# Kernel tuning notes

Measured on AMD Instinct MI355X. Metric: run time of the kernel, lower is better.

The kernel has to match this reference:

```python
import jax, jax.numpy as jnp
import numpy as np

DIM = 384
NHEAD = 8
HD = DIM // NHEAD          # 48, rotary/pos-enc head dim
P = 3
CORR_DIM = 2 * 49 * P * P  # 882
NFRAMES = 24
PPI = 96                   # patches per frame
NPATCH = NFRAMES * PPI     # 2304 SoftAgg segments (unique kk)
E = NPATCH * NFRAMES       # 55296 edges
M = PPI                    # tokens per (i,j) group


def _linear(x, W, b):
    return x @ W + b


def _ln(x, g, b, eps=1e-3):
    mu = x.mean(-1, keepdims=True)
    var = ((x - mu) ** 2).mean(-1, keepdims=True)
    return (x - mu) * jax.lax.rsqrt(var + eps) * g + b


def _mlp2(x, W1, b1, W2, b2):
    return _linear(jax.nn.relu(_linear(x, W1, b1)), W2, b2)


@jax.custom_vjp
def grad_clip(x):
    return x

def _gc_fwd(x):
    return x, None

def _gc_bwd(_, g):
    g = jnp.where(jnp.isnan(g), jnp.zeros_like(g), g)
    return (jnp.clip(g, -0.01, 0.01),)

grad_clip.defvjp(_gc_fwd, _gc_bwd)


def _soft_agg(x, seg, Wf, bf, Wg, bg, Wh, bh):
    # x: [1,E,D]; seg: [E] contiguous segment ids in [0, NPATCH)
    g = _linear(x, Wg, bg)[0]                                    # [E,D]
    gmax = jax.ops.segment_max(g, seg, num_segments=NPATCH)
    ex = jnp.exp(g - gmax[seg])
    den = jax.ops.segment_sum(ex, seg, num_segments=NPATCH)
    w = ex / den[seg]                                            # scatter_softmax over segments
    f = _linear(x, Wf, bf)[0]
    y = jax.ops.segment_sum(f * w, seg, num_segments=NPATCH)     # [NPATCH,D]
    return _linear(y, Wh, bh)[seg][None]                         # expand back to [1,E,D]


def _rotate_half(x):
    x1, x2 = jnp.split(x, 2, axis=-1)
    return jnp.concatenate([-x2, x1], axis=-1)


def _gated_linear_attention(x, cos, sin, Wq, bq, Wk, bk, Wv, bv, Wm, bm, Wgt, bgt):
    # x: [N,M,D]; cos/sin: [N,1,M,HD] broadcast over heads
    N = x.shape[0]
    def heads(t):
        return t.reshape(N, M, NHEAD, HD).transpose(0, 2, 1, 3)  # [N,H,M,HD]
    q = heads(_linear(x, Wq, bq))
    k = heads(_linear(x, Wk, bk))
    v = heads(_linear(x, Wv, bv))
    q = q * cos + _rotate_half(q) * sin
    k = k * cos + _rotate_half(k) * sin
    Q = jax.nn.elu(q) + 1.0
    K = jax.nn.elu(k) + 1.0
    KV = jnp.einsum('nhsd,nhsv->nhdv', K, v)
    Z = 1.0 / (jnp.einsum('nhld,nhd->nhl', Q, K.sum(2)) + 1e-6)
    out = jnp.einsum('nhld,nhdv,nhl->nhlv', Q, KV, Z)
    msg = _linear(out.transpose(0, 2, 1, 3).reshape(N, M, DIM), Wm, bm)
    gate = jax.nn.sigmoid(_linear(jnp.concatenate([x, msg], -1), Wgt, bgt))
    return x + gate * msg


def _forward(net, inp, corr, posenc_cache, kk, ix, jx, ij_ind,
             Wc1, bc1, Wc2, bc2, g_lnc, b_lnc, Wc3, bc3,
             g_norm, b_norm,
             W1a, b1a, W1b, b1b, W2a, b2a, W2b, b2b,
             Wf, bf, Wg, bg, Wh, bh,
             g_norm2, b_norm2,
             Wq, bq, Wk, bk, Wv, bv, Wm, bm, Wgt, bgt,
             Wd, bd, Ww, bw):
    # corr encoder: Linear-ReLU-Linear-LN-ReLU-Linear
    c = jax.nn.relu(_linear(corr, Wc1, bc1))
    c = _ln(_linear(c, Wc2, bc2), g_lnc, b_lnc)
    c = _linear(jax.nn.relu(c), Wc3, bc3)
    net = net + inp + c
    net = _ln(net, g_norm, b_norm)
    # neighbor gather + masked MLP + residual (mask applied BEFORE the MLP, as in torch)
    mask_ix = (ix >= 0).astype(net.dtype)[None, :, None]
    mask_jx = (jx >= 0).astype(net.dtype)[None, :, None]
    net = net + _mlp2(mask_ix * net[:, ix], W1a, b1a, W1b, b1b)
    net = net + _mlp2(mask_jx * net[:, jx], W2a, b2a, W2b, b2b)
    net = net + _soft_agg(net, kk, Wf, bf, Wg, bg, Wh, bh)
    b = net.shape[0]
    flat = ij_ind.reshape(-1)
    tokens = net[:, flat, :].reshape(-1, M, DIM)                 # [N,M,D], N = E//M
    pe = posenc_cache[:, :, :, flat, :].reshape(2, tokens.shape[0], 1, M, HD)
    tokens = _ln(tokens, g_norm2, b_norm2)
    tokens = _gated_linear_attention(tokens, pe[0], pe[1], Wq, bq, Wk, bk, Wv, bv, Wm, bm, Wgt, bgt)
    tokens = tokens.reshape(b, -1, DIM)
    reverse_ind = jnp.zeros((E,), jnp.int32).at[flat].set(jnp.arange(E, dtype=jnp.int32))
    net = tokens[:, reverse_ind, :]
    d_out = grad_clip(_linear(jax.nn.relu(net), Wd, bd))
    w_out = jax.nn.sigmoid(grad_clip(_linear(jax.nn.relu(net), Ww, bw)))
    return net, d_out, w_out


def setup_inputs() -> dict:
    key = jax.random.key(0)
    ki = iter(jax.random.split(key, 80))
    # complete patch graph: each patch connects to all frames; edge id = k*NFRAMES + j
    kkn = np.repeat(np.arange(NPATCH), NFRAMES)
    iin = kkn // PPI
    jjn = np.tile(np.arange(NFRAMES), NPATCH)
    e = np.arange(E)
    ixn = np.where(jjn >= 1, e - 1, -1)                 # fastba.neighbors: same kk, jj-1
    jxn = np.where(jjn + 1 < NFRAMES, e + 1, -1)        # same kk, jj+1
    ij = iin * 12345 + jjn
    ij_ind = np.sort(np.argsort(ij, kind='stable').reshape(-1, M), axis=-1)

    def rn(shape):
        return jax.random.normal(next(ki), shape, jnp.float32)
    def W(fi, fo):
        s = 1.0 / np.sqrt(fi)
        return jax.random.uniform(next(ki), (fi, fo), jnp.float32, -s, s)
    def bvec(fi, n):
        s = 1.0 / np.sqrt(fi)
        return jax.random.uniform(next(ki), (n,), jnp.float32, -s, s)

    theta = jax.random.uniform(next(ki), (1, 1, E, HD), jnp.float32, 0.0, 2.0 * np.pi)
    posenc = jnp.stack([jnp.cos(theta), jnp.sin(theta)], axis=0)  # [2,1,1,E,HD]

    return {
        'net': rn((1, E, DIM)), 'inp': rn((1, E, DIM)),
        'corr': rn((1, E, CORR_DIM)), 'flow': rn((1, E, 2)),
        'posenc_cache': posenc,
        'ii': jnp.asarray(iin, jnp.int32), 'jj': jnp.asarray(jjn, jnp.int32),
        'kk': jnp.asarray(kkn, jnp.int32), 'ix': jnp.asarray(ixn, jnp.int32),
        'jx': jnp.asarray(jxn, jnp.int32), 'ij_ind': jnp.asarray(ij_ind, jnp.int32),
        'Wc1': W(CORR_DIM, DIM), 'bc1': bvec(CORR_DIM, DIM),
        'Wc2': W(DIM, DIM), 'bc2': bvec(DIM, DIM),
        'g_lnc': jnp.ones((DIM,), jnp.float32), 'b_lnc': jnp.zeros((DIM,), jnp.float32),
        'Wc3': W(DIM, DIM), 'bc3': bvec(DIM, DIM),
        'g_norm': jnp.ones((DIM,), jnp.float32), 'b_norm': jnp.zeros((DIM,), jnp.float32),
        'W1a': W(DIM, DIM), 'b1a': bvec(DIM, DIM), 'W1b': W(DIM, DIM), 'b1b': bvec(DIM, DIM),
        'W2a': W(DIM, DIM), 'b2a': bvec(DIM, DIM), 'W2b': W(DIM, DIM), 'b2b': bvec(DIM, DIM),
        'Wf': W(DIM, DIM), 'bf': bvec(DIM, DIM), 'Wg': W(DIM, DIM), 'bg': bvec(DIM, DIM),
        'Wh': W(DIM, DIM), 'bh': bvec(DIM, DIM),
        'g_norm2': jnp.ones((DIM,), jnp.float32), 'b_norm2': jnp.zeros((DIM,), jnp.float32),
        'Wq': W(DIM, DIM), 'bq': bvec(DIM, DIM), 'Wk': W(DIM, DIM), 'bk': bvec(DIM, DIM),
        'Wv': W(DIM, DIM), 'bv': bvec(DIM, DIM), 'Wm': W(DIM, DIM), 'bm': bvec(DIM, DIM),
        'Wgt': W(2 * DIM, DIM), 'bgt': bvec(2 * DIM, DIM),
        'Wd': W(DIM, 2), 'bd': bvec(DIM, 2), 'Ww': W(DIM, 2), 'bw': bvec(DIM, 2),
    }


def reference(net, inp, corr, flow, posenc_cache, ii, jj, kk, ix, jx, ij_ind,
              Wc1, bc1, Wc2, bc2, g_lnc, b_lnc, Wc3, bc3,
              g_norm, b_norm,
              W1a, b1a, W1b, b1b, W2a, b2a, W2b, b2b,
              Wf, bf, Wg, bg, Wh, bh,
              g_norm2, b_norm2,
              Wq, bq, Wk, bk, Wv, bv, Wm, bm, Wgt, bgt,
              Wd, bd, Ww, bw):
    return _forward(net, inp, corr, posenc_cache, kk, ix, jx, ij_ind,
                    Wc1, bc1, Wc2, bc2, g_lnc, b_lnc, Wc3, bc3,
                    g_norm, b_norm,
                    W1a, b1a, W1b, b1b, W2a, b2a, W2b, b2b,
                    Wf, bf, Wg, bg, Wh, bh,
                    g_norm2, b_norm2,
                    Wq, bq, Wk, bk, Wv, bv, Wm, bm, Wgt, bgt,
                    Wd, bd, Ww, bw)
```

## Files before the change

### kernel.cpp

```cpp
#include <hip/hip_runtime.h>
#include <math.h>

#define DIMV 384
#define NHEADV 8
#define HDV 48
#define CORR_DIMV 882
#define CORR_PAD 896
#define NFRAMESV 24
#define PPIV 96
#define NPATCHV (NFRAMESV * PPIV)
#define ETOK (NPATCHV * NFRAMESV)
#define MTOK 96
#define NGRP (ETOK / MTOK)

using f32x4 = __attribute__((ext_vector_type(4))) float;
using s16x8 = __attribute__((ext_vector_type(8))) short;
using u16x4 = __attribute__((ext_vector_type(4))) unsigned short;

__device__ __forceinline__ unsigned int f2bf(float x) {
    union { float f; unsigned int u; } c; c.f = x;
    unsigned int u = c.u;
    u += 0x7fffu + ((u >> 16) & 1u);
    return u >> 16;
}
__device__ __forceinline__ float bf2f(unsigned short x) {
    union { unsigned int u; float f; } c; c.u = ((unsigned int)x) << 16;
    return c.f;
}

__device__ __forceinline__ void gload_lds16(const void* g, void* l) {
    __builtin_amdgcn_global_load_lds(
        (const __attribute__((address_space(1))) unsigned int*)g,
        (__attribute__((address_space(3))) unsigned int*)l, 16, 0, 0);
}

__device__ __forceinline__ void xcd_tile(int& colblk, int& rowblk) {
    const int nwg  = gridDim.x * gridDim.y;
    const int flat = blockIdx.y * gridDim.x + blockIdx.x;
    const int xcd  = flat & 7;
    const int base = flat >> 3;
    const int q = nwg >> 3, r = nwg & 7;
    const int nf = (xcd < r ? xcd * (q + 1) : r * (q + 1) + (xcd - r) * q) + base;
    colblk = nf % gridDim.x;
    rowblk = nf / gridDim.x;
}

template<int EPI, bool GATHER>
__global__ __launch_bounds__(256)
void gemm_bb(const unsigned short* __restrict__ A, int lda,
             const unsigned short* __restrict__ Wt,
             const float* __restrict__ bias,
             float* __restrict__ C,
             unsigned short* __restrict__ Cb, int ldcb, int cbofs,
             const int* __restrict__ gidx,
             const unsigned short* __restrict__ zrow, int K)
{
    int colblk, rowblk;
    xcd_tile(colblk, rowblk);
    const int row0 = rowblk * 128;
    const int col0 = colblk * 128;

    __shared__ __align__(16) unsigned short As[128 * 32];
    __shared__ __align__(16) unsigned short Bs[128 * 32];

    const int tid  = threadIdx.x;
    const int lane = tid & 63;
    const int wid  = tid >> 6;
    const int wm   = wid >> 1;
    const int wn   = wid & 1;

    const int rl = lane >> 2;
    const int cp = lane & 3;

    const unsigned short* asrc[2];
    const unsigned short* bsrc[2];
    #pragma unroll
    for (int s = 0; s < 2; ++s) {
        const int r = wid * 32 + s * 16 + rl;
        const int c = cp ^ ((r >> 1) & 3);
        long arow = row0 + r;
        if (GATHER) arow = gidx[row0 + r];
        asrc[s] = (GATHER && arow < 0) ? (zrow + c * 8)
                                       : (A + arow * (long)lda + c * 8);
        bsrc[s] = Wt + (long)(col0 + r) * K + c * 8;
    }
    unsigned short* adst[2] = { &As[(wid * 32) * 32], &As[(wid * 32 + 16) * 32] };
    unsigned short* bdst[2] = { &Bs[(wid * 32) * 32], &Bs[(wid * 32 + 16) * 32] };

    f32x4 acc[4][4] = {};
    const int ntiles = K >> 5;

    for (int t = 0; t < ntiles; ++t) {
        const int ko = t * 32;
        gload_lds16(asrc[0] + ko, adst[0]);
        gload_lds16(asrc[1] + ko, adst[1]);
        gload_lds16(bsrc[0] + ko, bdst[0]);
        gload_lds16(bsrc[1] + ko, bdst[1]);
        __syncthreads();

        const int rsel = lane & 15;
        const int kq   = lane >> 4;
        s16x8 a[4], b[4];
        #pragma unroll
        for (int i = 0; i < 4; ++i) {
            const int R = wm * 64 + i * 16 + rsel;
            a[i] = *(const s16x8*)&As[R * 32 + ((kq ^ ((R >> 1) & 3)) << 3)];
        }
        #pragma unroll
        for (int j = 0; j < 4; ++j) {
            const int R = wn * 64 + j * 16 + rsel;
            b[j] = *(const s16x8*)&Bs[R * 32 + ((kq ^ ((R >> 1) & 3)) << 3)];
        }
        #pragma unroll
        for (int i = 0; i < 4; ++i)
            #pragma unroll
            for (int j = 0; j < 4; ++j)
                acc[i][j] = __builtin_amdgcn_mfma_f32_16x16x32_bf16(a[i], b[j], acc[i][j], 0, 0, 0);
        __syncthreads();
    }

    const int ccol = lane & 15;
    const int rgrp = lane >> 4;
    #pragma unroll
    for (int i = 0; i < 4; ++i) {
        const long rbase = row0 + wm * 64 + i * 16 + rgrp * 4;
        #pragma unroll
        for (int j = 0; j < 4; ++j) {
            const int col = col0 + wn * 64 + j * 16 + ccol;
            const float bsv = bias ? bias[col] : 0.f;
            #pragma unroll
            for (int rr = 0; rr < 4; ++rr) {
                const long row = rbase + rr;
                float v = acc[i][j][rr] + bsv;
                if (EPI == 0) C[row * (long)DIMV + col] = v;
                if (EPI == 1) Cb[row * (long)ldcb + cbofs + col] = (unsigned short)f2bf(fmaxf(v, 0.f));
                if (EPI == 3) { const long off = row * (long)DIMV + col;
                                const float nv = C[off] + v;
                                C[off] = nv; Cb[row * (long)ldcb + col] = (unsigned short)f2bf(nv); }
                if (EPI == 5) Cb[row * (long)ldcb + cbofs + col] = (unsigned short)f2bf(v);
                if (EPI == 7) {
                    const float gate = 1.f / (1.f + expf(-v));
                    const float tok  = bf2f(Cb[row * (long)ldcb + col]);
                    const float msg  = bf2f(Cb[row * (long)ldcb + cbofs + col]);
                    C[(long)gidx[row] * DIMV + col] = tok + gate * msg;
                }
            }
        }
    }
}

struct WPtrs13 { const float* p[13]; };

__global__ __launch_bounds__(256)
void wtrans13(WPtrs13 w, unsigned short* __restrict__ out)
{
    __shared__ float t[32][33];
    const float* W = w.p[blockIdx.z];
    unsigned short* O = out + (size_t)blockIdx.z * DIMV * DIMV;
    const int k0 = blockIdx.x * 32, n0 = blockIdx.y * 32;
    const int tx = threadIdx.x, ty = threadIdx.y;
    #pragma unroll
    for (int i = ty; i < 32; i += 8)
        t[i][tx] = W[(long)(k0 + i) * DIMV + n0 + tx];
    __syncthreads();
    #pragma unroll
    for (int i = ty; i < 32; i += 8)
        O[(long)(n0 + i) * DIMV + k0 + tx] = (unsigned short)f2bf(t[tx][i]);
}

__global__ __launch_bounds__(256)
void wtransb(const float* __restrict__ W, unsigned short* __restrict__ O,
             int krows, int ldo)
{
    __shared__ float t[32][33];
    const int k0 = blockIdx.x * 32, n0 = blockIdx.y * 32;
    const int tx = threadIdx.x, ty = threadIdx.y;
    #pragma unroll
    for (int i = ty; i < 32; i += 8)
        t[i][tx] = (k0 + i < krows) ? W[(long)(k0 + i) * DIMV + n0 + tx] : 0.f;
    __syncthreads();
    #pragma unroll
    for (int i = ty; i < 32; i += 8)
        O[(long)(n0 + i) * ldo + k0 + tx] = (unsigned short)f2bf(t[tx][i]);
}

__global__ __launch_bounds__(256)
void corrconv(const float* __restrict__ corr, unsigned int* __restrict__ corrb,
              unsigned int* __restrict__ zr)
{
    if (blockIdx.x == 0 && threadIdx.x < 512) zr[threadIdx.x] = 0u;
    const long idx = (long)blockIdx.x * 256 + threadIdx.x;
    if (idx >= (long)ETOK * (CORR_PAD / 2)) return;
    const long e = idx / (CORR_PAD / 2);
    const int  p = (int)(idx % (CORR_PAD / 2));
    const int  k = p * 2;
    unsigned v = 0u;
    if (k + 1 < CORR_DIMV) {
        const float2 f = *(const float2*)(corr + e * CORR_DIMV + k);
        v = f2bf(f.x) | (f2bf(f.y) << 16);
    }
    corrb[idx] = v;
}

template<int MODE, bool RELUB>
__global__ __launch_bounds__(256)
void ln_kernel(float* __restrict__ dst, unsigned short* __restrict__ dstb, int ldb,
               const float* __restrict__ s0, const float* __restrict__ s1,
               const unsigned short* __restrict__ sb,
               const float* __restrict__ seg, const int* __restrict__ gather,
               const float* __restrict__ g, const float* __restrict__ b)
{
    const int wave = threadIdx.x >> 6;
    const int lane = threadIdx.x & 63;
    const long row = (long)blockIdx.x * 4 + wave;
    const long srow = (MODE == 2) ? (long)gather[row] : row;

    float x[6];
    float sum = 0.f;
    #pragma unroll
    for (int i = 0; i < 6; ++i) {
        int c = lane + i * 64;
        float v;
        if (MODE == 0) v = bf2f(sb[srow * DIMV + c]);
        if (MODE == 1) v = s0[srow * DIMV + c] + s1[srow * DIMV + c] + bf2f(sb[srow * DIMV + c]);
        if (MODE == 2) v = s0[srow * DIMV + c] + seg[(srow / NFRAMESV) * DIMV + c];
        x[i] = v; sum += v;
    }
    #pragma unroll
    for (int o = 32; o > 0; o >>= 1) sum += __shfl_xor(sum, o);
    float mu = sum * (1.f / DIMV);
    float vs = 0.f;
    #pragma unroll
    for (int i = 0; i < 6; ++i) { float d = x[i] - mu; vs += d * d; }
    #pragma unroll
    for (int o = 32; o > 0; o >>= 1) vs += __shfl_xor(vs, o);
    float rstd = rsqrtf(vs * (1.f / DIMV) + 1e-3f);
    #pragma unroll
    for (int i = 0; i < 6; ++i) {
        int c = lane + i * 64;
        float y = (x[i] - mu) * rstd * g[c] + b[c];
        if (dst)  dst[row * DIMV + c] = y;
        if (dstb) dstb[row * (long)ldb + c] =
            (unsigned short)f2bf(RELUB ? fmaxf(y, 0.f) : y);
    }
}

__global__ __launch_bounds__(384)
void softagg_kernel(const unsigned short* __restrict__ gbuf,
                    const unsigned short* __restrict__ fbuf,
                    unsigned short* __restrict__ yb)
{
    const int p = blockIdx.x;
    const int col = threadIdx.x;
    const long base = (long)p * NFRAMESV * DIMV + col;
    float gv[NFRAMESV];
    float gmax = -INFINITY;
    #pragma unroll
    for (int r = 0; r < NFRAMESV; ++r) {
        gv[r] = bf2f(gbuf[base + (long)r * DIMV]);
        gmax = fmaxf(gmax, gv[r]);
    }
    float den = 0.f;
    #pragma unroll
    for (int r = 0; r < NFRAMESV; ++r) { gv[r] = expf(gv[r] - gmax); den += gv[r]; }
    float acc = 0.f;
    #pragma unroll
    for (int r = 0; r < NFRAMESV; ++r) acc += bf2f(fbuf[base + (long)r * DIMV]) * gv[r];
    yb[(long)p * DIMV + col] = (unsigned short)f2bf(acc / den);
}

__global__ __launch_bounds__(256)
void rope_kernel(unsigned short* __restrict__ q, unsigned short* __restrict__ k,
                 const float* __restrict__ pos, const int* __restrict__ flat)
{
    const long idx = (long)blockIdx.x * 256 + threadIdx.x;
    const long e = idx / 48;
    const int rem = (int)(idx % 48);
    const int h = rem / 6, d4 = (rem % 6) * 4;
    const int tok = flat[e];
    const float* cp = pos + (long)tok * HDV;
    const float* sp = pos + (long)ETOK * HDV + (long)tok * HDV;
    const float4 c1 = *(const float4*)(cp + d4);
    const float4 c2 = *(const float4*)(cp + d4 + 24);
    const float4 s1 = *(const float4*)(sp + d4);
    const float4 s2 = *(const float4*)(sp + d4 + 24);
    const long o1 = e * DIMV + h * HDV + d4;
    const long o2 = o1 + 24;

    float c1a[4] = {c1.x, c1.y, c1.z, c1.w};
    float c2a[4] = {c2.x, c2.y, c2.z, c2.w};
    float s1a[4] = {s1.x, s1.y, s1.z, s1.w};
    float s2a[4] = {s2.x, s2.y, s2.z, s2.w};

    u16x4 q1 = *(const u16x4*)&q[o1];
    u16x4 q2 = *(const u16x4*)&q[o2];
    u16x4 k1 = *(const u16x4*)&k[o1];
    u16x4 k2 = *(const u16x4*)&k[o2];
    u16x4 q1o, q2o, k1o, k2o;
    #pragma unroll
    for (int i = 0; i < 4; ++i) {
        const float qa = bf2f(q1[i]), qb = bf2f(q2[i]);
        float r1 = qa * c1a[i] - qb * s1a[i];
        float r2 = qb * c2a[i] + qa * s2a[i];
        r1 = (r1 > 0.f) ? r1 + 1.f : expf(r1);
        r2 = (r2 > 0.f) ? r2 + 1.f : expf(r2);
        q1o[i] = (unsigned short)f2bf(r1);
        q2o[i] = (unsigned short)f2bf(r2);
        const float ka = bf2f(k1[i]), kb = bf2f(k2[i]);
        float t1 = ka * c1a[i] - kb * s1a[i];
        float t2 = kb * c2a[i] + ka * s2a[i];
        t1 = (t1 > 0.f) ? t1 + 1.f : expf(t1);
        t2 = (t2 > 0.f) ? t2 + 1.f : expf(t2);
        k1o[i] = (unsigned short)f2bf(t1);
        k2o[i] = (unsigned short)f2bf(t2);
    }
    *(u16x4*)&q[o1] = q1o;
    *(u16x4*)&q[o2] = q2o;
    *(u16x4*)&k[o1] = k1o;
    *(u16x4*)&k[o2] = k2o;
}

__global__ __launch_bounds__(256)
void attn_kernel(const unsigned short* __restrict__ qb,
                 const unsigned short* __restrict__ kb,
                 const unsigned short* __restrict__ vb,
                 unsigned short* __restrict__ ob)
{
    __shared__ unsigned short KVt[4][48][64];
    __shared__ float KsumS[4][48];
    __shared__ float ZlS[4][96];

    const int tid  = threadIdx.x;
    const int wid  = tid >> 6;
    const int lane = tid & 63;
    const int task = blockIdx.x * 4 + wid;
    const int n = task >> 3, h = task & 7;

    const long base = ((long)n * MTOK) * DIMV + h * HDV;

    const int c16   = lane & 15;
    const int kq    = lane >> 4;
    const int khalf = kq * 8;

    if (lane < 48) {
        const int s = (lane & 7) << 3;
        const uint4 z = make_uint4(0u, 0u, 0u, 0u);
        *(uint4*)&KVt[wid][lane][48 ^ s] = z;
        *(uint4*)&KVt[wid][lane][56 ^ s] = z;
    }

    f32x4 kv[3][3] = {};
    float ksum_p[3] = {0.f, 0.f, 0.f};

    for (int ks = 0; ks < 3; ++ks) {
        const int l0 = ks * 32 + khalf;
        s16x8 afr[3], bfr[3];
        #pragma unroll
        for (int mf = 0; mf < 3; ++mf) {
            const int d = mf * 16 + c16;
            union { unsigned short us[8]; s16x8 v; } pk;
            float s = 0.f;
            #pragma unroll
            for (int j = 0; j < 8; ++j) {
                const unsigned short kw = kb[base + (long)(l0 + j) * DIMV + d];
                s += bf2f(kw);
                pk.us[j] = kw;
            }
            ksum_p[mf] += s;
            afr[mf] = pk.v;
        }
        #pragma unroll
        for (int nf = 0; nf < 3; ++nf) {
            const int dv = nf * 16 + c16;
            union { unsigned short us[8]; s16x8 v; } pk;
            #pragma unroll
            for (int j = 0; j < 8; ++j)
                pk.us[j] = vb[base + (long)(l0 + j) * DIMV + dv];
            bfr[nf] = pk.v;
        }
        #pragma unroll
        for (int mf = 0; mf < 3; ++mf)
            #pragma unroll
            for (int nf = 0; nf < 3; ++nf)
                kv[mf][nf] = __builtin_amdgcn_mfma_f32_16x16x32_bf16(afr[mf], bfr[nf], kv[mf][nf], 0, 0, 0);
    }

    #pragma unroll
    for (int mf = 0; mf < 3; ++mf) {
        float s = ksum_p[mf];
        s += __shfl_xor(s, 16);
        s += __shfl_xor(s, 32);
        if (kq == 0) KsumS[wid][mf * 16 + c16] = s;
    }

    #pragma unroll
    for (int mf = 0; mf < 3; ++mf) {
        #pragma unroll
        for (int nf = 0; nf < 3; ++nf) {
            const int dv = nf * 16 + c16;
            const int d0 = (mf * 16 + kq * 4) ^ ((dv & 7) << 3);
            uint2 w;
            w.x = f2bf(kv[mf][nf][0]) | (f2bf(kv[mf][nf][1]) << 16);
            w.y = f2bf(kv[mf][nf][2]) | (f2bf(kv[mf][nf][3]) << 16);
            *(uint2*)&KVt[wid][dv][d0] = w;
        }
    }

    s16x8 qf[6][2];
    const s16x8 zfrag = {0, 0, 0, 0, 0, 0, 0, 0};
    #pragma unroll
    for (int mf = 0; mf < 6; ++mf) {
        const int l = mf * 16 + c16;
        float dsum = 0.f;
        #pragma unroll
        for (int ks = 0; ks < 2; ++ks) {
            if (ks == 0 || kq < 2) {
                const int d = ks * 32 + khalf;
                union { unsigned short us[8]; s16x8 v; } pk;
                pk.v = *(const s16x8*)&qb[base + (long)l * DIMV + d];
                #pragma unroll
                for (int j = 0; j < 8; ++j)
                    dsum += bf2f(pk.us[j]) * KsumS[wid][d + j];
                qf[mf][ks] = pk.v;
            } else {
                qf[mf][ks] = zfrag;
            }
        }
        dsum += __shfl_xor(dsum, 16);
        dsum += __shfl_xor(dsum, 32);
        if (kq == 0) ZlS[wid][l] = 1.f / (dsum + 1e-6f);
    }

    #pragma unroll
    for (int nf = 0; nf < 3; ++nf) {
        const int dv = nf * 16 + c16;
        const int sw = (dv & 7) << 3;
        const s16x8 b0 = *(const s16x8*)&KVt[wid][dv][khalf ^ sw];
        const s16x8 b1 = *(const s16x8*)&KVt[wid][dv][(32 + khalf) ^ sw];
        #pragma unroll
        for (int mf = 0; mf < 6; ++mf) {
            f32x4 a = {};
            a = __builtin_amdgcn_mfma_f32_16x16x32_bf16(qf[mf][0], b0, a, 0, 0, 0);
            a = __builtin_amdgcn_mfma_f32_16x16x32_bf16(qf[mf][1], b1, a, 0, 0, 0);
            const int lb = mf * 16 + kq * 4;
            const long rbase = base + (long)lb * DIMV + dv;
            #pragma unroll
            for (int rr = 0; rr < 4; ++rr) {
                const float z = ZlS[wid][lb + rr];
                ob[rbase + (long)rr * DIMV] = (unsigned short)f2bf(a[rr] * z);
            }
        }
    }
}

__global__ __launch_bounds__(256)
void head_kernel(const float* __restrict__ net,
                 const float* __restrict__ Wd, const float* __restrict__ bd,
                 const float* __restrict__ Ww, const float* __restrict__ bw,
                 float* __restrict__ dout, float* __restrict__ wout)
{
    const int wave = threadIdx.x >> 6;
    const int lane = threadIdx.x & 63;
    const long row = (long)blockIdx.x * 4 + wave;
    const float* p = net + row * DIMV;
    float a0 = 0.f, a1 = 0.f, a2 = 0.f, a3 = 0.f;
    #pragma unroll
    for (int i = 0; i < 6; ++i) {
        int c = lane + i * 64;
        float r = fmaxf(p[c], 0.f);
        a0 = fmaf(r, Wd[c * 2 + 0], a0);
        a1 = fmaf(r, Wd[c * 2 + 1], a1);
        a2 = fmaf(r, Ww[c * 2 + 0], a2);
        a3 = fmaf(r, Ww[c * 2 + 1], a3);
    }
    #pragma unroll
    for (int o = 32; o > 0; o >>= 1) {
        a0 += __shfl_xor(a0, o);
        a1 += __shfl_xor(a1, o);
        a2 += __shfl_xor(a2, o);
        a3 += __shfl_xor(a3, o);
    }
    if (lane == 0) {
        dout[row * 2 + 0] = a0 + bd[0];
        dout[row * 2 + 1] = a1 + bd[1];
        wout[row * 2 + 0] = 1.f / (1.f + expf(-(a2 + bw[0])));
        wout[row * 2 + 1] = 1.f / (1.f + expf(-(a3 + bw[1])));
    }
}

extern "C" void kernel_launch(void* const* d_in, const int* in_sizes, int n_in,
                              void* d_out, int out_size, void* d_ws, size_t ws_size,
                              hipStream_t stream)
{
    const float* net_in = (const float*)d_in[0];
    const float* inp    = (const float*)d_in[1];
    const float* corr   = (const float*)d_in[2];
    const float* posenc = (const float*)d_in[4];
    const int*   ix     = (const int*)d_in[8];
    const int*   jx     = (const int*)d_in[9];
    const int*   flat   = (const int*)d_in[10];

    const float* Wc1 = (const float*)d_in[11]; const float* bc1 = (const float*)d_in[12];
    const float* Wc2 = (const float*)d_in[13]; const float* bc2 = (const float*)d_in[14];
    const float* g_lnc = (const float*)d_in[15]; const float* b_lnc = (const float*)d_in[16];
    const float* Wc3 = (const float*)d_in[17]; const float* bc3 = (const float*)d_in[18];
    const float* g_norm = (const float*)d_in[19]; const float* b_norm = (const float*)d_in[20];
    const float* W1a = (const float*)d_in[21]; const float* b1a = (const float*)d_in[22];
    const float* W1b = (const float*)d_in[23]; const float* b1b = (const float*)d_in[24];
    const float* W2a = (const float*)d_in[25]; const float* b2a = (const float*)d_in[26];
    const float* W2b = (const float*)d_in[27]; const float* b2b = (const float*)d_in[28];
    const float* Wf = (const float*)d_in[29]; const float* bff = (const float*)d_in[30];
    const float* Wg = (const float*)d_in[31]; const float* bg = (const float*)d_in[32];
    const float* Wh = (const float*)d_in[33]; const float* bh = (const float*)d_in[34];
    const float* g_norm2 = (const float*)d_in[35]; const float* b_norm2 = (const float*)d_in[36];
    const float* Wq = (const float*)d_in[37]; const float* bq = (const float*)d_in[38];
    const float* Wk = (const float*)d_in[39]; const float* bk = (const float*)d_in[40];
    const float* Wv = (const float*)d_in[41]; const float* bv = (const float*)d_in[42];
    const float* Wm = (const float*)d_in[43]; const float* bm = (const float*)d_in[44];
    const float* Wgt = (const float*)d_in[45]; const float* bgt = (const float*)d_in[46];
    const float* Wd = (const float*)d_in[47]; const float* bd = (const float*)d_in[48];
    const float* Ww = (const float*)d_in[49]; const float* bw = (const float*)d_in[50];

    const size_t EB  = (size_t)ETOK * DIMV;
    const size_t WSLOT = (size_t)DIMV * DIMV;
    char* p = (char*)d_ws;
    float* X0  = (float*)p;           p += EB * 4;
    float* Y2f = (float*)p;           p += (size_t)NPATCHV * DIMV * 4;
    unsigned short* WT = (unsigned short*)p;
    p += (13 * WSLOT + (size_t)DIMV * CORR_PAD + (size_t)DIMV * 768) * 2;
    unsigned short* ZR  = (unsigned short*)p; p += 4096;
    unsigned short* Cb0 = (unsigned short*)p; p += EB * 2;
    unsigned short* Bb  = (unsigned short*)p; p += EB * 2;
    unsigned short* Xb1 = (unsigned short*)p; p += EB * 2;
    unsigned short* Xb2 = (unsigned short*)p; p += EB * 2;
    unsigned short* TM  = (unsigned short*)p; p += (size_t)ETOK * 768 * 2;
    unsigned short* Yb  = (unsigned short*)p; p += (size_t)NPATCHV * DIMV * 2;
    unsigned short* qb  = (unsigned short*)p; p += EB * 2;
    unsigned short* kb  = (unsigned short*)p; p += EB * 2;
    unsigned short* vb  = (unsigned short*)p; p += EB * 2;
    unsigned short* corrb = qb;

    unsigned short* Wc2t = WT + 0 * WSLOT;
    unsigned short* Wc3t = WT + 1 * WSLOT;
    unsigned short* W1at = WT + 2 * WSLOT;
    unsigned short* W1bt = WT + 3 * WSLOT;
    unsigned short* W2at = WT + 4 * WSLOT;
    unsigned short* W2bt = WT + 5 * WSLOT;
    unsigned short* Wft  = WT + 6 * WSLOT;
    unsigned short* Wgt_ = WT + 7 * WSLOT;
    unsigned short* Wht  = WT + 8 * WSLOT;
    unsigned short* Wqt  = WT + 9 * WSLOT;
    unsigned short* Wkt  = WT + 10 * WSLOT;
    unsigned short* Wvt  = WT + 11 * WSLOT;
    unsigned short* Wmt  = WT + 12 * WSLOT;
    unsigned short* Wc1t = WT + 13 * WSLOT;
    unsigned short* Wgtt = Wc1t + (size_t)DIMV * CORR_PAD;

    float* out_net = (float*)d_out;
    float* out_d = out_net + EB;
    float* out_w = out_d + (size_t)ETOK * 2;

    const dim3 gB(DIMV / 128, ETOK / 128);
    const dim3 gY(DIMV / 128, NPATCHV / 128);
    const int lnBlocks = ETOK / 4;

    {
        const long tot = (long)ETOK * (CORR_PAD / 2);
        corrconv<<<(int)((tot + 255) / 256), 256, 0, stream>>>(corr, (unsigned int*)corrb, (unsigned int*)ZR);
    }
    {
        WPtrs13 w;
        w.p[0] = Wc2; w.p[1] = Wc3; w.p[2] = W1a; w.p[3] = W1b; w.p[4] = W2a;
        w.p[5] = W2b; w.p[6] = Wf;  w.p[7] = Wg;  w.p[8] = Wh;  w.p[9] = Wq;
        w.p[10] = Wk; w.p[11] = Wv; w.p[12] = Wm;
        wtrans13<<<dim3(12, 12, 13), dim3(32, 8), 0, stream>>>(w, WT);
        wtransb<<<dim3(28, 12), dim3(32, 8), 0, stream>>>(Wc1, Wc1t, CORR_DIMV, CORR_PAD);
        wtransb<<<dim3(24, 12), dim3(32, 8), 0, stream>>>(Wgt, Wgtt, 768, 768);
    }

    gemm_bb<1, false><<<gB, 256, 0, stream>>>(corrb, CORR_PAD, Wc1t, bc1, nullptr, Cb0, DIMV, 0, nullptr, ZR, CORR_PAD);
    gemm_bb<5, false><<<gB, 256, 0, stream>>>(Cb0, DIMV, Wc2t, bc2, nullptr, Xb1, DIMV, 0, nullptr, ZR, DIMV);
    ln_kernel<0, true><<<lnBlocks, 256, 0, stream>>>(nullptr, Cb0, DIMV, nullptr, nullptr, Xb1, nullptr, nullptr, g_lnc, b_lnc);
    gemm_bb<5, false><<<gB, 256, 0, stream>>>(Cb0, DIMV, Wc3t, bc3, nullptr, Xb2, DIMV, 0, nullptr, ZR, DIMV);

    ln_kernel<1, false><<<lnBlocks, 256, 0, stream>>>(X0, Bb, DIMV, net_in, inp, Xb2, nullptr, nullptr, g_norm, b_norm);

    gemm_bb<1, true><<<gB, 256, 0, stream>>>(Bb, DIMV, W1at, b1a, nullptr, Cb0, DIMV, 0, ix, ZR, DIMV);
    gemm_bb<3, false><<<gB, 256, 0, stream>>>(Cb0, DIMV, W1bt, b1b, X0, Bb, DIMV, 0, nullptr, ZR, DIMV);

    gemm_bb<1, true><<<gB, 256, 0, stream>>>(Bb, DIMV, W2at, b2a, nullptr, Cb0, DIMV, 0, jx, ZR, DIMV);
    gemm_bb<3, false><<<gB, 256, 0, stream>>>(Cb0, DIMV, W2bt, b2b, X0, Bb, DIMV, 0, nullptr, ZR, DIMV);

    gemm_bb<5, false><<<gB, 256, 0, stream>>>(Bb, DIMV, Wgt_, bg, nullptr, Xb1, DIMV, 0, nullptr, ZR, DIMV);
    gemm_bb<5, false><<<gB, 256, 0, stream>>>(Bb, DIMV, Wft, bff, nullptr, Xb2, DIMV, 0, nullptr, ZR, DIMV);
    softagg_kernel<<<NPATCHV, 384, 0, stream>>>(Xb1, Xb2, Yb);
    gemm_bb<0, false><<<gY, 256, 0, stream>>>(Yb, DIMV, Wht, bh, Y2f, nullptr, DIMV, 0, nullptr, ZR, DIMV);

    ln_kernel<2, false><<<lnBlocks, 256, 0, stream>>>(nullptr, TM, 768, X0, nullptr, nullptr, Y2f, flat, g_norm2, b_norm2);

    gemm_bb<5, false><<<gB, 256, 0, stream>>>(TM, 768, Wqt, bq, nullptr, qb, DIMV, 0, nullptr, ZR, DIMV);
    gemm_bb<5, false><<<gB, 256, 0, stream>>>(TM, 768, Wkt, bk, nullptr, kb, DIMV, 0, nullptr, ZR, DIMV);
    gemm_bb<5, false><<<gB, 256, 0, stream>>>(TM, 768, Wvt, bv, nullptr, vb, DIMV, 0, nullptr, ZR, DIMV);

    rope_kernel<<<(int)((long)ETOK * 48 / 256), 256, 0, stream>>>(qb, kb, posenc, flat);

    attn_kernel<<<NGRP * NHEADV / 4, 256, 0, stream>>>(qb, kb, vb, Cb0);

    gemm_bb<5, false><<<gB, 256, 0, stream>>>(Cb0, DIMV, Wmt, bm, nullptr, TM, 768, 384, nullptr, ZR, DIMV);

    gemm_bb<7, false><<<gB, 256, 0, stream>>>(TM, 768, Wgtt, bgt, out_net, TM, 768, 384, flat, ZR, 768);

    head_kernel<<<lnBlocks, 256, 0, stream>>>(out_net, Wd, bd, Ww, bw, out_d, out_w);
}
```

Before: 1.007 ms.

## Double-buffer GEMM LDS, fuse QKV and gate/feature GEMMs, drop fp32 residual

The GEMM main loop now uses two LDS buffers. The next K-tile's global-to-LDS loads are issued before computing on the current tile, with one barrier pair per iteration instead of a load-then-compute sync pattern. The Q/K/V projections are merged into one 1152-wide GEMM, and the gate/feature projections into one 768-wide GEMM, with concatenated biases and strided consumers. The fp32 residual buffer X0 is removed so residual updates accumulate in bf16 in place. This cuts launches, A-operand rereads and fp32 traffic, at the risk of extra bf16 rounding in the residual path.

Result: faster. 882.5 us (median of 2 runs) (-12.3%).

```diff
diff --git a/kernel.cpp b/kernel.cpp
--- a/kernel.cpp
+++ b/kernel.cpp
@@ -60,8 +60,8 @@
     const int row0 = rowblk * 128;
     const int col0 = colblk * 128;
 
-    __shared__ __align__(16) unsigned short As[128 * 32];
-    __shared__ __align__(16) unsigned short Bs[128 * 32];
+    __shared__ __align__(16) unsigned short As[2 * 128 * 32];
+    __shared__ __align__(16) unsigned short Bs[2 * 128 * 32];
 
     const int tid  = threadIdx.x;
     const int lane = tid & 63;
@@ -84,40 +84,52 @@
                                        : (A + arow * (long)lda + c * 8);
         bsrc[s] = Wt + (long)(col0 + r) * K + c * 8;
     }
-    unsigned short* adst[2] = { &As[(wid * 32) * 32], &As[(wid * 32 + 16) * 32] };
-    unsigned short* bdst[2] = { &Bs[(wid * 32) * 32], &Bs[(wid * 32 + 16) * 32] };
 
     f32x4 acc[4][4] = {};
     const int ntiles = K >> 5;
-
-    for (int t = 0; t < ntiles; ++t) {
-        const int ko = t * 32;
-        gload_lds16(asrc[0] + ko, adst[0]);
-        gload_lds16(asrc[1] + ko, adst[1]);
-        gload_lds16(bsrc[0] + ko, bdst[0]);
-        gload_lds16(bsrc[1] + ko, bdst[1]);
-        __syncthreads();
-
-        const int rsel = lane & 15;
-        const int kq   = lane >> 4;
-        s16x8 a[4], b[4];
+    const int rsel = lane & 15;
+    const int kq   = lane >> 4;
+
+    auto stage = [&](int b, int ko) {
+        unsigned short* a0 = &As[b * 4096 + wid * 1024];
+        unsigned short* b0 = &Bs[b * 4096 + wid * 1024];
+        gload_lds16(asrc[0] + ko, a0);
+        gload_lds16(asrc[1] + ko, a0 + 512);
+        gload_lds16(bsrc[0] + ko, b0);
+        gload_lds16(bsrc[1] + ko, b0 + 512);
+    };
+    auto body = [&](int b) {
+        const unsigned short* Ab = &As[b * 4096];
+        const unsigned short* Bf = &Bs[b * 4096];
+        s16x8 a[4], w[4];
         #pragma unroll
         for (int i = 0; i < 4; ++i) {
             const int R = wm * 64 + i * 16 + rsel;
-            a[i] = *(const s16x8*)&As[R * 32 + ((kq ^ ((R >> 1) & 3)) << 3)];
+            a[i] = *(const s16x8*)&Ab[R * 32 + ((kq ^ ((R >> 1) & 3)) << 3)];
         }
         #pragma unroll
         for (int j = 0; j < 4; ++j) {
             const int R = wn * 64 + j * 16 + rsel;
-            b[j] = *(const s16x8*)&Bs[R * 32 + ((kq ^ ((R >> 1) & 3)) << 3)];
+            w[j] = *(const s16x8*)&Bf[R * 32 + ((kq ^ ((R >> 1) & 3)) << 3)];
         }
         #pragma unroll
         for (int i = 0; i < 4; ++i)
             #pragma unroll
             for (int j = 0; j < 4; ++j)
-                acc[i][j] = __builtin_amdgcn_mfma_f32_16x16x32_bf16(a[i], b[j], acc[i][j], 0, 0, 0);
-        __syncthreads();
-    }
+                acc[i][j] = __builtin_amdgcn_mfma_f32_16x16x32_bf16(a[i], w[j], acc[i][j], 0, 0, 0);
+    };
+
+    stage(0, 0);
+    int cur = 0;
+    for (int t = 0; t + 1 < ntiles; ++t) {
+        stage(cur ^ 1, (t + 1) << 5);
+        asm volatile("s_waitcnt vmcnt(4)\n\ts_barrier" ::: "memory");
+        body(cur);
+        asm volatile("s_barrier" ::: "memory");
+        cur ^= 1;
+    }
+    asm volatile("s_waitcnt vmcnt(0)\n\ts_barrier" ::: "memory");
+    body(cur);
 
     const int ccol = lane & 15;
     const int rgrp = lane >> 4;
@@ -134,10 +146,9 @@
                 float v = acc[i][j][rr] + bsv;
                 if (EPI == 0) C[row * (long)DIMV + col] = v;
                 if (EPI == 1) Cb[row * (long)ldcb + cbofs + col] = (unsigned short)f2bf(fmaxf(v, 0.f));
-                if (EPI == 3) { const long off = row * (long)DIMV + col;
-                                const float nv = C[off] + v;
-                                C[off] = nv; Cb[row * (long)ldcb + col] = (unsigned short)f2bf(nv); }
                 if (EPI == 5) Cb[row * (long)ldcb + cbofs + col] = (unsigned short)f2bf(v);
+                if (EPI == 6) { const long off = row * (long)ldcb + col;
+                                Cb[off] = (unsigned short)f2bf(bf2f(Cb[off]) + v); }
                 if (EPI == 7) {
                     const float gate = 1.f / (1.f + expf(-v));
                     const float tok  = bf2f(Cb[row * (long)ldcb + col]);
@@ -202,9 +213,21 @@
     corrb[idx] = v;
 }
 
+__global__ __launch_bounds__(256)
+void biascat(const float* __restrict__ bq, const float* __restrict__ bk,
+             const float* __restrict__ bv, const float* __restrict__ bg,
+             const float* __restrict__ bf_, float* __restrict__ bqkv,
+             float* __restrict__ bgf)
+{
+    const int t = blockIdx.x * 256 + threadIdx.x;
+    if (t < 384)       { bqkv[t] = bq[t];       bgf[t] = bg[t]; }
+    else if (t < 768)  { bqkv[t] = bk[t - 384]; bgf[t] = bf_[t - 384]; }
+    else if (t < 1152) { bqkv[t] = bv[t - 768]; }
+}
+
 template<int MODE, bool RELUB>
 __global__ __launch_bounds__(256)
-void ln_kernel(float* __restrict__ dst, unsigned short* __restrict__ dstb, int ldb,
+void ln_kernel(unsigned short* __restrict__ dstb, int ldb,
                const float* __restrict__ s0, const float* __restrict__ s1,
                const unsigned short* __restrict__ sb,
                const float* __restrict__ seg, const int* __restrict__ gather,
@@ -223,7 +246,7 @@
         float v;
         if (MODE == 0) v = bf2f(sb[srow * DIMV + c]);
         if (MODE == 1) v = s0[srow * DIMV + c] + s1[srow * DIMV + c] + bf2f(sb[srow * DIMV + c]);
-        if (MODE == 2) v = s0[srow * DIMV + c] + seg[(srow / NFRAMESV) * DIMV + c];
+        if (MODE == 2) v = bf2f(sb[srow * DIMV + c]) + seg[(srow / NFRAMESV) * DIMV + c];
         x[i] = v; sum += v;
     }
     #pragma unroll
@@ -239,25 +262,22 @@
     for (int i = 0; i < 6; ++i) {
         int c = lane + i * 64;
         float y = (x[i] - mu) * rstd * g[c] + b[c];
-        if (dst)  dst[row * DIMV + c] = y;
-        if (dstb) dstb[row * (long)ldb + c] =
-            (unsigned short)f2bf(RELUB ? fmaxf(y, 0.f) : y);
+        dstb[row * (long)ldb + c] = (unsigned short)f2bf(RELUB ? fmaxf(y, 0.f) : y);
     }
 }
 
 __global__ __launch_bounds__(384)
-void softagg_kernel(const unsigned short* __restrict__ gbuf,
-                    const unsigned short* __restrict__ fbuf,
+void softagg_kernel(const unsigned short* __restrict__ gf,
                     unsigned short* __restrict__ yb)
 {
     const int p = blockIdx.x;
     const int col = threadIdx.x;
-    const long base = (long)p * NFRAMESV * DIMV + col;
+    const long base = (long)p * NFRAMESV * 768 + col;
     float gv[NFRAMESV];
     float gmax = -INFINITY;
     #pragma unroll
     for (int r = 0; r < NFRAMESV; ++r) {
-        gv[r] = bf2f(gbuf[base + (long)r * DIMV]);
+        gv[r] = bf2f(gf[base + (long)r * 768]);
         gmax = fmaxf(gmax, gv[r]);
     }
     float den = 0.f;
@@ -265,13 +285,13 @@
     for (int r = 0; r < NFRAMESV; ++r) { gv[r] = expf(gv[r] - gmax); den += gv[r]; }
     float acc = 0.f;
     #pragma unroll
-    for (int r = 0; r < NFRAMESV; ++r) acc += bf2f(fbuf[base + (long)r * DIMV]) * gv[r];
+    for (int r = 0; r < NFRAMESV; ++r) acc += bf2f(gf[base + 384 + (long)r * 768]) * gv[r];
     yb[(long)p * DIMV + col] = (unsigned short)f2bf(acc / den);
 }
 
 __global__ __launch_bounds__(256)
 void rope_kernel(unsigned short* __restrict__ q, unsigned short* __restrict__ k,
-                 const float* __restrict__ pos, const int* __restrict__ flat)
+                 int ld, const float* __restrict__ pos, const int* __restrict__ flat)
 {
     const long idx = (long)blockIdx.x * 256 + threadIdx.x;
     const long e = idx / 48;
@@ -284,7 +304,7 @@
     const float4 c2 = *(const float4*)(cp + d4 + 24);
     const float4 s1 = *(const float4*)(sp + d4);
     const float4 s2 = *(const float4*)(sp + d4 + 24);
-    const long o1 = e * DIMV + h * HDV + d4;
+    const long o1 = e * ld + h * HDV + d4;
     const long o2 = o1 + 24;
 
     float c1a[4] = {c1.x, c1.y, c1.z, c1.w};
@@ -323,8 +343,8 @@
 __global__ __launch_bounds__(256)
 void attn_kernel(const unsigned short* __restrict__ qb,
                  const unsigned short* __restrict__ kb,
-                 const unsigned short* __restrict__ vb,
-                 unsigned short* __restrict__ ob)
+                 const unsigned short* __restrict__ vb, int ld,
+                 unsigned short* __restrict__ ob, int ldo)
 {
     __shared__ unsigned short KVt[4][48][64];
     __shared__ float KsumS[4][48];
@@ -336,7 +356,8 @@
     const int task = blockIdx.x * 4 + wid;
     const int n = task >> 3, h = task & 7;
 
-    const long base = ((long)n * MTOK) * DIMV + h * HDV;
+    const long base  = ((long)n * MTOK) * ld + h * HDV;
+    const long baseo = ((long)n * MTOK) * ldo + h * HDV;
 
     const int c16   = lane & 15;
     const int kq    = lane >> 4;
@@ -362,7 +383,7 @@
             float s = 0.f;
             #pragma unroll
             for (int j = 0; j < 8; ++j) {
-                const unsigned short kw = kb[base + (long)(l0 + j) * DIMV + d];
+                const unsigned short kw = kb[base + (long)(l0 + j) * ld + d];
                 s += bf2f(kw);
                 pk.us[j] = kw;
             }
@@ -375,7 +396,7 @@
             union { unsigned short us[8]; s16x8 v; } pk;
             #pragma unroll
             for (int j = 0; j < 8; ++j)
-                pk.us[j] = vb[base + (long)(l0 + j) * DIMV + dv];
+                pk.us[j] = vb[base + (long)(l0 + j) * ld + dv];
             bfr[nf] = pk.v;
         }
         #pragma unroll
@@ -417,7 +438,7 @@
             if (ks == 0 || kq < 2) {
                 const int d = ks * 32 + khalf;
                 union { unsigned short us[8]; s16x8 v; } pk;
-                pk.v = *(const s16x8*)&qb[base + (long)l * DIMV + d];
+                pk.v = *(const s16x8*)&qb[base + (long)l * ld + d];
                 #pragma unroll
                 for (int j = 0; j < 8; ++j)
                     dsum += bf2f(pk.us[j]) * KsumS[wid][d + j];
@@ -443,11 +464,11 @@
             a = __builtin_amdgcn_mfma_f32_16x16x32_bf16(qf[mf][0], b0, a, 0, 0, 0);
             a = __builtin_amdgcn_mfma_f32_16x16x32_bf16(qf[mf][1], b1, a, 0, 0, 0);
             const int lb = mf * 16 + kq * 4;
-            const long rbase = base + (long)lb * DIMV + dv;
+            const long rbase = baseo + (long)lb * ldo + dv;
             #pragma unroll
             for (int rr = 0; rr < 4; ++rr) {
                 const float z = ZlS[wid][lb + rr];
-                ob[rbase + (long)rr * DIMV] = (unsigned short)f2bf(a[rr] * z);
+                ob[rbase + (long)rr * ldo] = (unsigned short)f2bf(a[rr] * z);
             }
         }
     }
@@ -524,21 +545,21 @@
     const size_t EB  = (size_t)ETOK * DIMV;
     const size_t WSLOT = (size_t)DIMV * DIMV;
     char* p = (char*)d_ws;
-    float* X0  = (float*)p;           p += EB * 4;
     float* Y2f = (float*)p;           p += (size_t)NPATCHV * DIMV * 4;
     unsigned short* WT = (unsigned short*)p;
     p += (13 * WSLOT + (size_t)DIMV * CORR_PAD + (size_t)DIMV * 768) * 2;
     unsigned short* ZR  = (unsigned short*)p; p += 4096;
+    float* bqkv = (float*)p;          p += 1152 * 4;
+    float* bgf  = (float*)p;          p += 768 * 4;
     unsigned short* Cb0 = (unsigned short*)p; p += EB * 2;
     unsigned short* Bb  = (unsigned short*)p; p += EB * 2;
     unsigned short* Xb1 = (unsigned short*)p; p += EB * 2;
     unsigned short* Xb2 = (unsigned short*)p; p += EB * 2;
+    unsigned short* Xgf = (unsigned short*)p; p += (size_t)ETOK * 768 * 2;
     unsigned short* TM  = (unsigned short*)p; p += (size_t)ETOK * 768 * 2;
     unsigned short* Yb  = (unsigned short*)p; p += (size_t)NPATCHV * DIMV * 2;
-    unsigned short* qb  = (unsigned short*)p; p += EB * 2;
-    unsigned short* kb  = (unsigned short*)p; p += EB * 2;
-    unsigned short* vb  = (unsigned short*)p; p += EB * 2;
-    unsigned short* corrb = qb;
+    unsigned short* QKV = (unsigned short*)p; p += (size_t)ETOK * 1152 * 2;
+    unsigned short* corrb = QKV;
 
     unsigned short* Wc2t = WT + 0 * WSLOT;
     unsigned short* Wc3t = WT + 1 * WSLOT;
@@ -546,12 +567,9 @@
     unsigned short* W1bt = WT + 3 * WSLOT;
     unsigned short* W2at = WT + 4 * WSLOT;
     unsigned short* W2bt = WT + 5 * WSLOT;
-    unsigned short* Wft  = WT + 6 * WSLOT;
-    unsigned short* Wgt_ = WT + 7 * WSLOT;
+    unsigned short* WgfT = WT + 6 * WSLOT;
     unsigned short* Wht  = WT + 8 * WSLOT;
-    unsigned short* Wqt  = WT + 9 * WSLOT;
-    unsigned short* Wkt  = WT + 10 * WSLOT;
-    unsigned short* Wvt  = WT + 11 * WSLOT;
+    unsigned short* Wqkv = WT + 9 * WSLOT;
     unsigned short* Wmt  = WT + 12 * WSLOT;
     unsigned short* Wc1t = WT + 13 * WSLOT;
     unsigned short* Wgtt = Wc1t + (size_t)DIMV * CORR_PAD;
@@ -561,6 +579,8 @@
     float* out_w = out_d + (size_t)ETOK * 2;
 
     const dim3 gB(DIMV / 128, ETOK / 128);
+    const dim3 gGF(768 / 128, ETOK / 128);
+    const dim3 gQKV(1152 / 128, ETOK / 128);
     const dim3 gY(DIMV / 128, NPATCHV / 128);
     const int lnBlocks = ETOK / 4;
 
@@ -571,40 +591,38 @@
     {
         WPtrs13 w;
         w.p[0] = Wc2; w.p[1] = Wc3; w.p[2] = W1a; w.p[3] = W1b; w.p[4] = W2a;
-        w.p[5] = W2b; w.p[6] = Wf;  w.p[7] = Wg;  w.p[8] = Wh;  w.p[9] = Wq;
+        w.p[5] = W2b; w.p[6] = Wg;  w.p[7] = Wf;  w.p[8] = Wh;  w.p[9] = Wq;
         w.p[10] = Wk; w.p[11] = Wv; w.p[12] = Wm;
         wtrans13<<<dim3(12, 12, 13), dim3(32, 8), 0, stream>>>(w, WT);
         wtransb<<<dim3(28, 12), dim3(32, 8), 0, stream>>>(Wc1, Wc1t, CORR_DIMV, CORR_PAD);
         wtransb<<<dim3(24, 12), dim3(32, 8), 0, stream>>>(Wgt, Wgtt, 768, 768);
+        biascat<<<5, 256, 0, stream>>>(bq, bk, bv, bg, bff, bqkv, bgf);
     }
 
     gemm_bb<1, false><<<gB, 256, 0, stream>>>(corrb, CORR_PAD, Wc1t, bc1, nullptr, Cb0, DIMV, 0, nullptr, ZR, CORR_PAD);
     gemm_bb<5, false><<<gB, 256, 0, stream>>>(Cb0, DIMV, Wc2t, bc2, nullptr, Xb1, DIMV, 0, nullptr, ZR, DIMV);
-    ln_kernel<0, true><<<lnBlocks, 256, 0, stream>>>(nullptr, Cb0, DIMV, nullptr, nullptr, Xb1, nullptr, nullptr, g_lnc, b_lnc);
+    ln_kernel<0, true><<<lnBlocks, 256, 0, stream>>>(Cb0, DIMV, nullptr, nullptr, Xb1, nullptr, nullptr, g_lnc, b_lnc);
     gemm_bb<5, false><<<gB, 256, 0, stream>>>(Cb0, DIMV, Wc3t, bc3, nullptr, Xb2, DIMV, 0, nullptr, ZR, DIMV);
 
-    ln_kernel<1, false><<<lnBlocks, 256, 0, stream>>>(X0, Bb, DIMV, net_in, inp, Xb2, nullptr, nullptr, g_norm, b_norm);
+    ln_kernel<1, false><<<lnBlocks, 256, 0, stream>>>(Bb, DIMV, net_in, inp, Xb2, nullptr, nullptr, g_norm, b_norm);
 
     gemm_bb<1, true><<<gB, 256, 0, stream>>>(Bb, DIMV, W1at, b1a, nullptr, Cb0, DIMV, 0, ix, ZR, DIMV);
-    gemm_bb<3, false><<<gB, 256, 0, stream>>>(Cb0, DIMV, W1bt, b1b, X0, Bb, DIMV, 0, nullptr, ZR, DIMV);
+    gemm_bb<6, false><<<gB, 256, 0, stream>>>(Cb0, DIMV, W1bt, b1b, nullptr, Bb, DIMV, 0, nullptr, ZR, DIMV);
 
     gemm_bb<1, true><<<gB, 256, 0, stream>>>(Bb, DIMV, W2at, b2a, nullptr, Cb0, DIMV, 0, jx, ZR, DIMV);
-    gemm_bb<3, false><<<gB, 256, 0, stream>>>(Cb0, DIMV, W2bt, b2b, X0, Bb, DIMV, 0, nullptr, ZR, DIMV);
-
-    gemm_bb<5, false><<<gB, 256, 0, stream>>>(Bb, DIMV, Wgt_, bg, nullptr, Xb1, DIMV, 0, nullptr, ZR, DIMV);
-    gemm_bb<5, false><<<gB, 256, 0, stream>>>(Bb, DIMV, Wft, bff, nullptr, Xb2, DIMV, 0, nullptr, ZR, DIMV);
-    softagg_kernel<<<NPATCHV, 384, 0, stream>>>(Xb1, Xb2, Yb);
+    gemm_bb<6, false><<<gB, 256, 0, stream>>>(Cb0, DIMV, W2bt, b2b, nullptr, Bb, DIMV, 0, nullptr, ZR, DIMV);
+
+    gemm_bb<5, false><<<gGF, 256, 0, stream>>>(Bb, DIMV, WgfT, bgf, nullptr, Xgf, 768, 0, nullptr, ZR, DIMV);
+    softagg_kernel<<<NPATCHV, 384, 0, stream>>>(Xgf, Yb);
     gemm_bb<0, false><<<gY, 256, 0, stream>>>(Yb, DIMV, Wht, bh, Y2f, nullptr, DIMV, 0, nullptr, ZR, DIMV);
 
-    ln_kernel<2, false><<<lnBlocks, 256, 0, stream>>>(nullptr, TM, 768, X0, nullptr, nullptr, Y2f, flat, g_norm2, b_norm2);
-
-    gemm_bb<5, false><<<gB, 256, 0, stream>>>(TM, 768, Wqt, bq, nullptr, qb, DIMV, 0, nullptr, ZR, DIMV);
-    gemm_bb<5, false><<<gB, 256, 0, stream>>>(TM, 768, Wkt, bk, nullptr, kb, DIMV, 0, nullptr, ZR, DIMV);
-    gemm_bb<5, false><<<gB, 256, 0, stream>>>(TM, 768, Wvt, bv, nullptr, vb, DIMV, 0, nullptr, ZR, DIMV);
-
-    rope_kernel<<<(int)((long)ETOK * 48 / 256), 256, 0, stream>>>(qb, kb, posenc, flat);
-
-    attn_kernel<<<NGRP * NHEADV / 4, 256, 0, stream>>>(qb, kb, vb, Cb0);
+    ln_kernel<2, false><<<lnBlocks, 256, 0, stream>>>(TM, 768, nullptr, nullptr, Bb, Y2f, flat, g_norm2, b_norm2);
+
+    gemm_bb<5, false><<<gQKV, 256, 0, stream>>>(TM, 768, Wqkv, bqkv, nullptr, QKV, 1152, 0, nullptr, ZR, DIMV);
+
+    rope_kernel<<<(int)((long)ETOK * 48 / 256), 256, 0, stream>>>(QKV, QKV + 384, 1152, posenc, flat);
+
+    attn_kernel<<<NGRP * NHEADV / 4, 256, 0, stream>>>(QKV, QKV + 384, QKV + 768, 1152, Cb0, DIMV);
 
     gemm_bb<5, false><<<gB, 256, 0, stream>>>(Cb0, DIMV, Wmt, bm, nullptr, TM, 768, 384, nullptr, ZR, DIMV);
 
```
